# Kernel optimization log

Hardware: AMD Instinct MI355X
Metric: run time of the kernel (lower is better)

Reference implementation:

```python
import jax, jax.numpy as jnp
import numpy as np

R_CUT = 5.0
L_MAX = 3
N_MAX = (8, 7, 6, 5)  # n_max per angular order l (Laplacian-eigenstate-like, shrinking with l)
EPS = 1e-12


def _radial_basis(r):
    """r: [E] -> [E, N_MAX[0]] sine radial basis with smooth cosine cutoff.
    R_n(r) = f_cut(r) * sin((n+1) pi r / r_cut) / r, n = 0..n_max-1."""
    n = jnp.arange(1, N_MAX[0] + 1, dtype=r.dtype)  # (n+1)
    fcut = jnp.where(r < R_CUT, 0.5 * (jnp.cos(jnp.pi * r / R_CUT) + 1.0), 0.0)
    rb = jnp.sin(n[None, :] * (jnp.pi / R_CUT) * r[:, None]) / (r[:, None] + EPS)
    return rb * fcut[:, None]


def _spherical_harmonics(v, r):
    """v: [E,3], r: [E] -> tuple of real SH arrays ([E,1],[E,3],[E,5],[E,7]), m = -l..l."""
    ir = 1.0 / (r + EPS)
    x, y, z = v[:, 0] * ir, v[:, 1] * ir, v[:, 2] * ir
    pi = np.pi
    x2, y2, z2 = x * x, y * y, z * z
    # l = 0
    y0 = jnp.full_like(r, 0.5 * np.sqrt(1.0 / pi))[:, None]
    # l = 1
    c1 = np.sqrt(3.0 / (4.0 * pi))
    y1 = jnp.stack([c1 * y, c1 * z, c1 * x], axis=-1)
    # l = 2
    y2b = jnp.stack([
        0.5 * np.sqrt(15.0 / pi) * x * y,
        0.5 * np.sqrt(15.0 / pi) * y * z,
        0.25 * np.sqrt(5.0 / pi) * (2.0 * z2 - x2 - y2),
        0.5 * np.sqrt(15.0 / pi) * x * z,
        0.25 * np.sqrt(15.0 / pi) * (x2 - y2),
    ], axis=-1)
    # l = 3
    y3b = jnp.stack([
        0.25 * np.sqrt(35.0 / (2.0 * pi)) * y * (3.0 * x2 - y2),
        0.5 * np.sqrt(105.0 / pi) * x * y * z,
        0.25 * np.sqrt(21.0 / (2.0 * pi)) * y * (4.0 * z2 - x2 - y2),
        0.25 * np.sqrt(7.0 / pi) * z * (2.0 * z2 - 3.0 * x2 - 3.0 * y2),
        0.25 * np.sqrt(21.0 / (2.0 * pi)) * x * (4.0 * z2 - x2 - y2),
        0.25 * np.sqrt(105.0 / pi) * z * (x2 - y2),
        0.25 * np.sqrt(35.0 / (2.0 * pi)) * x * (x2 - 3.0 * y2),
    ], axis=-1)
    return (y0, y1, y2b, y3b)


def setup_inputs() -> dict:
    key = jax.random.key(0)
    E = 1_000_000
    vectors = 1.5 * jax.random.normal(key, (E, 3), dtype=jnp.float32)
    return {"vectors": vectors}


def reference(vectors):
    # vectors: [E, 3] bare cartesian edge vectors
    r = jnp.sqrt(jnp.sum(vectors * vectors, axis=-1))  # [E]
    rb = _radial_basis(r)                               # [E, N_MAX[0]]
    sh = _spherical_harmonics(vectors, r)               # per-l [E, 2l+1]
    # vector_expansion_l = radial_l[:, None, :] * sh_l[:, :, None] -> [E, 2l+1, n_max_l]
    blocks = tuple(sh[l][:, :, None] * rb[:, None, :N_MAX[l]] for l in range(L_MAX + 1))
    return blocks
```

## Files before the change

kernel.cpp:

```cpp
#include <hip/hip_runtime.h>
#include <math.h>


#define RCUT 5.0f
#define EPSF 1e-12f

typedef float fx4 __attribute__((ext_vector_type(4)));

__device__ __forceinline__ void radial(float rr, float ir, float rb[8]) {
  float theta = (3.14159265358979323846f / RCUT) * rr;
  float s = __sinf(theta);
  float c = __cosf(theta);
  float fcut = (rr < RCUT) ? 0.5f * (c + 1.0f) : 0.0f;
  float g = fcut * ir;
  float twoc = 2.0f * c;
  float sp = 0.0f, sn = s;
  rb[0] = sn * g;
#pragma unroll
  for (int n = 1; n < 8; ++n) {
    float s2 = twoc * sn - sp;
    sp = sn;
    sn = s2;
    rb[n] = sn * g;
  }
}

__global__ __launch_bounds__(256) void vexp_s0(const float* __restrict__ v,
                                               float* __restrict__ out,
                                               long long n4) {
  long long tid = (long long)blockIdx.x * blockDim.x + threadIdx.x;
  if (tid >= n4) return;
  long long e = tid >> 1;
  int half = (int)(tid & 1);
  float x = v[3 * e + 0], y = v[3 * e + 1], z = v[3 * e + 2];
  float rr = sqrtf(x * x + y * y + z * z);
  float ir = 1.0f / (rr + EPSF);
  float rb[8];
  radial(rr, ir, rb);
  const float y0c = 0.28209479177387814f;
  int o = 4 * half;
  fx4 val = {y0c * rb[o], y0c * rb[o + 1], y0c * rb[o + 2], y0c * rb[o + 3]};
  __builtin_nontemporal_store(val, &reinterpret_cast<fx4*>(out)[tid]);
}

template <int L>
__global__ __launch_bounds__(256) void vexp_sec(const float* __restrict__ v,
                                                float* __restrict__ secbase,
                                                int E) {
  constexpr int M = 2 * L + 1;
  constexpr int NM = 8 - L;
  constexpr int S = M * NM;
  __shared__ fx4 lbuf[4][16 * S];
  const int lane = threadIdx.x & 63;
  const int wave = threadIdx.x >> 6;
  const long long e0 = ((long long)blockIdx.x * 4 + wave) * 64;
  if (e0 >= E) return;
  const bool fullwave = (e0 + 64 <= (long long)E);
  const int e = (int)e0 + lane;
  const bool valid = e < E;

  float x = 0.0f, y = 0.0f, z = 0.0f;
  if (valid) {
    x = v[3 * (size_t)e + 0];
    y = v[3 * (size_t)e + 1];
    z = v[3 * (size_t)e + 2];
  }
  float rr = sqrtf(x * x + y * y + z * z);
  float ir = 1.0f / (rr + EPSF);
  float rb[8];
  radial(rr, ir, rb);

  float ux = x * ir, uy = y * ir, uz = z * ir;
  float xx = ux * ux, yy = uy * uy, zz = uz * uz;

  float sh[M];
  if constexpr (L == 1) {
    const float c1 = 0.48860251190291992f;
    sh[0] = c1 * uy;
    sh[1] = c1 * uz;
    sh[2] = c1 * ux;
  } else if constexpr (L == 2) {
    const float c2a = 1.09254843059207907f;
    const float c2b = 0.31539156525252001f;
    const float c2c = 0.54627421529603953f;
    sh[0] = c2a * ux * uy;
    sh[1] = c2a * uy * uz;
    sh[2] = c2b * (2.0f * zz - xx - yy);
    sh[3] = c2a * ux * uz;
    sh[4] = c2c * (xx - yy);
  } else {
    const float c3a = 0.59004358992664352f;
    const float c3b = 2.89061144264055405f;
    const float c3c = 0.45704579946446574f;
    const float c3d = 0.37317633259011546f;
    const float c3e = 1.44530572132027702f;
    sh[0] = c3a * uy * (3.0f * xx - yy);
    sh[1] = c3b * ux * uy * uz;
    sh[2] = c3c * uy * (4.0f * zz - xx - yy);
    sh[3] = c3d * uz * (2.0f * zz - 3.0f * xx - 3.0f * yy);
    sh[4] = c3c * ux * (4.0f * zz - xx - yy);
    sh[5] = c3e * uz * (xx - yy);
    sh[6] = c3a * ux * (xx - 3.0f * yy);
  }

  float vals[S];
#pragma unroll
  for (int m = 0; m < M; ++m)
#pragma unroll
    for (int n = 0; n < NM; ++n) vals[m * NM + n] = sh[m] * rb[n];

  if (fullwave) {
    float* lw = reinterpret_cast<float*>(lbuf[wave]);
#pragma unroll
    for (int i = 0; i < S; ++i) lw[lane * S + i] = vals[i];
    const fx4* l4 = lbuf[wave];
    fx4* g4 = reinterpret_cast<fx4*>(secbase + (size_t)e0 * S);
    constexpr int NF4 = 16 * S;
    constexpr int NITER = (NF4 + 63) / 64;
#pragma unroll
    for (int it = 0; it < NITER; ++it) {
      int k = lane + it * 64;
      if ((NF4 % 64 == 0) || k < NF4) __builtin_nontemporal_store(l4[k], &g4[k]);
    }
  } else if (valid) {
    float* o = secbase + (size_t)e * S;
#pragma unroll
    for (int i = 0; i < S; ++i) o[i] = vals[i];
  }
}

extern "C" void kernel_launch(void* const* d_in, const int* in_sizes, int n_in,
                              void* d_out, int out_size, void* d_ws, size_t ws_size,
                              hipStream_t stream) {
  const float* v = (const float*)d_in[0];
  float* out = (float*)d_out;
  int E = in_sizes[0] / 3;
  size_t E_ = (size_t)E;

  long long n4 = 2LL * E;
  int grid0 = (int)((n4 + 255) / 256);
  vexp_s0<<<grid0, 256, 0, stream>>>(v, out, n4);

  int waves = (E + 63) / 64;
  int grid = (waves + 3) / 4;
  vexp_sec<1><<<grid, 256, 0, stream>>>(v, out + 8 * E_, E);
  vexp_sec<2><<<grid, 256, 0, stream>>>(v, out + 29 * E_, E);
  vexp_sec<3><<<grid, 256, 0, stream>>>(v, out + 59 * E_, E);
}
```

Measured before the change: 74.67 us.

## Fuse four per-l expansion kernels into one launch with block-range dispatch

Merges the l=0 kernel and the three templated per-l section kernels into a single kernel whose blocks pick their section by block-index range, with one shared LDS buffer sized for the largest section. This removes three kernel launches and the gaps and tail drain between them, letting all sections overlap on the GPU. In exchange every block reserves the l=3 sized LDS (560 fx4 per wave), which may reduce occupancy for the smaller sections, and the l=0 blocks now each handle two strided chunks.

```diff
diff --git a/kernel.cpp b/kernel.cpp
--- a/kernel.cpp
+++ b/kernel.cpp
@@ -25,35 +25,15 @@
   }
 }
 
-__global__ __launch_bounds__(256) void vexp_s0(const float* __restrict__ v,
-                                               float* __restrict__ out,
-                                               long long n4) {
-  long long tid = (long long)blockIdx.x * blockDim.x + threadIdx.x;
-  if (tid >= n4) return;
-  long long e = tid >> 1;
-  int half = (int)(tid & 1);
-  float x = v[3 * e + 0], y = v[3 * e + 1], z = v[3 * e + 2];
-  float rr = sqrtf(x * x + y * y + z * z);
-  float ir = 1.0f / (rr + EPSF);
-  float rb[8];
-  radial(rr, ir, rb);
-  const float y0c = 0.28209479177387814f;
-  int o = 4 * half;
-  fx4 val = {y0c * rb[o], y0c * rb[o + 1], y0c * rb[o + 2], y0c * rb[o + 3]};
-  __builtin_nontemporal_store(val, &reinterpret_cast<fx4*>(out)[tid]);
-}
-
 template <int L>
-__global__ __launch_bounds__(256) void vexp_sec(const float* __restrict__ v,
-                                                float* __restrict__ secbase,
-                                                int E) {
+__device__ __forceinline__ void do_section(const float* __restrict__ v,
+                                           float* __restrict__ secbase, int E,
+                                           int task, fx4* __restrict__ l4,
+                                           int lane, int wave) {
   constexpr int M = 2 * L + 1;
   constexpr int NM = 8 - L;
   constexpr int S = M * NM;
-  __shared__ fx4 lbuf[4][16 * S];
-  const int lane = threadIdx.x & 63;
-  const int wave = threadIdx.x >> 6;
-  const long long e0 = ((long long)blockIdx.x * 4 + wave) * 64;
+  const long long e0 = ((long long)task * 4 + wave) * 64;
   if (e0 >= E) return;
   const bool fullwave = (e0 + 64 <= (long long)E);
   const int e = (int)e0 + lane;
@@ -110,22 +90,60 @@
     for (int n = 0; n < NM; ++n) vals[m * NM + n] = sh[m] * rb[n];
 
   if (fullwave) {
-    float* lw = reinterpret_cast<float*>(lbuf[wave]);
+    float* lw = reinterpret_cast<float*>(l4);
 #pragma unroll
     for (int i = 0; i < S; ++i) lw[lane * S + i] = vals[i];
-    const fx4* l4 = lbuf[wave];
     fx4* g4 = reinterpret_cast<fx4*>(secbase + (size_t)e0 * S);
     constexpr int NF4 = 16 * S;
     constexpr int NITER = (NF4 + 63) / 64;
 #pragma unroll
     for (int it = 0; it < NITER; ++it) {
       int k = lane + it * 64;
-      if ((NF4 % 64 == 0) || k < NF4) __builtin_nontemporal_store(l4[k], &g4[k]);
+      if ((NF4 % 64 == 0) || k < NF4)
+        __builtin_nontemporal_store(l4[k], &g4[k]);
     }
   } else if (valid) {
     float* o = secbase + (size_t)e * S;
 #pragma unroll
     for (int i = 0; i < S; ++i) o[i] = vals[i];
+  }
+}
+
+__global__ __launch_bounds__(256) void vexp_fused(const float* __restrict__ v,
+                                                  float* __restrict__ out,
+                                                  int E, int gsec) {
+  __shared__ fx4 lbuf[4][560];
+  const int bid = blockIdx.x;
+  const int lane = threadIdx.x & 63;
+  const int wave = threadIdx.x >> 6;
+  const size_t E_ = (size_t)E;
+
+  if (bid < gsec) {
+    const long long n4 = 2LL * E;
+    const float y0c = 0.28209479177387814f;
+#pragma unroll
+    for (int k = 0; k < 2; ++k) {
+      long long t = (long long)bid * 256 + threadIdx.x + (long long)k * gsec * 256;
+      if (t < n4) {
+        long long e = t >> 1;
+        int half = (int)(t & 1);
+        float x = v[3 * e + 0], y = v[3 * e + 1], z = v[3 * e + 2];
+        float rr = sqrtf(x * x + y * y + z * z);
+        float ir = 1.0f / (rr + EPSF);
+        float rb[8];
+        radial(rr, ir, rb);
+        int o = 4 * half;
+        fx4 val = {y0c * rb[o], y0c * rb[o + 1], y0c * rb[o + 2],
+                   y0c * rb[o + 3]};
+        __builtin_nontemporal_store(val, &reinterpret_cast<fx4*>(out)[t]);
+      }
+    }
+  } else if (bid < 2 * gsec) {
+    do_section<1>(v, out + 8 * E_, E, bid - gsec, lbuf[wave], lane, wave);
+  } else if (bid < 3 * gsec) {
+    do_section<2>(v, out + 29 * E_, E, bid - 2 * gsec, lbuf[wave], lane, wave);
+  } else {
+    do_section<3>(v, out + 59 * E_, E, bid - 3 * gsec, lbuf[wave], lane, wave);
   }
 }
 
@@ -135,15 +153,7 @@
   const float* v = (const float*)d_in[0];
   float* out = (float*)d_out;
   int E = in_sizes[0] / 3;
-  size_t E_ = (size_t)E;
-
-  long long n4 = 2LL * E;
-  int grid0 = (int)((n4 + 255) / 256);
-  vexp_s0<<<grid0, 256, 0, stream>>>(v, out, n4);
-
   int waves = (E + 63) / 64;
-  int grid = (waves + 3) / 4;
-  vexp_sec<1><<<grid, 256, 0, stream>>>(v, out + 8 * E_, E);
-  vexp_sec<2><<<grid, 256, 0, stream>>>(v, out + 29 * E_, E);
-  vexp_sec<3><<<grid, 256, 0, stream>>>(v, out + 59 * E_, E);
+  int gsec = (waves + 3) / 4;
+  vexp_fused<<<4 * gsec, 256, 0, stream>>>(v, out, E, gsec);
 }
```

Result: no change. 73.35 us (median of 2 runs) (-1.8%).
